# Optimization experiments

Hardware: AMD Instinct MI355X
Metric: run time of the kernel (lower is better)

## Reference

```python
import jax, jax.numpy as jnp
import numpy as np

N_NODES = 500000
D = 128          # input_dim
UNITS = 128
K = 32           # neigh_max
B = 20000        # batch of target nodes
LEAKY_ALPHA = 0.2  # tf.nn.leaky_relu default


def setup_inputs() -> dict:
    key = jax.random.key(0)
    k1, k2, k3, k4, k5, k6, k7 = jax.random.split(key, 7)
    features = jax.random.normal(k1, (N_NODES, D), dtype=jnp.float32)
    node = jax.random.randint(k2, (B, 1), 0, N_NODES, dtype=jnp.int32)
    neighbours = jax.random.randint(k3, (B, K), 0, N_NODES, dtype=jnp.int32)
    # learned parameters (glorot-scale random)
    kernel = jax.random.normal(k4, (1, D, D), dtype=jnp.float32) * (1.0 / np.sqrt(D))
    kernel1 = jax.random.normal(k5, (1, D, D), dtype=jnp.float32) * (1.0 / np.sqrt(D))
    attention_weights = jax.random.normal(k6, (1, 2 * D), dtype=jnp.float32) * (1.0 / np.sqrt(2 * D))
    neigh_weights = jax.random.normal(k7, (D, UNITS), dtype=jnp.float32) * (1.0 / np.sqrt(D))
    return {
        "features": features,
        "node": node,
        "neighbours": neighbours,
        "kernel": kernel,
        "kernel1": kernel1,
        "attention_weights": attention_weights,
        "neigh_weights": neigh_weights,
    }


def reference(features, node, neighbours, kernel, kernel1, attention_weights, neigh_weights):
    # gather: node_feat [B,1,D], neigh_feat [B,K,D]
    node_feat = features[node]
    neigh_feat = features[neighbours]
    # per-node projections (kernel tiled over batch in original == shared matmul)
    node_h = jnp.einsum('bkd,de->bke', node_feat, kernel[0])    # [B,1,D]
    neigh_h = jnp.einsum('bkd,de->bke', neigh_feat, kernel1[0])  # [B,K,D]
    # concat [neigh, tiled node] -> [B,K,2D]
    tile_node = jnp.broadcast_to(node_h, neigh_h.shape)
    concat_feat = jnp.concatenate([neigh_h, tile_node], axis=2)
    # attention score: [B,K,2D] @ [2D,1] -> [B,K,1], leaky_relu (alpha=0.2)
    score = concat_feat @ attention_weights.reshape(2 * D, 1)
    score = jnp.where(score > 0, score, LEAKY_ALPHA * score)
    # softmax over neighbors (axis K)
    final_score = jax.nn.softmax(score, axis=1)                  # [B,K,1]
    # weighted aggregate: neigh_h^T @ score -> [B,D]
    attention_feat = jnp.einsum('bkd,bk->bd', neigh_h, final_score[..., 0])
    # output projection
    return attention_feat @ neigh_weights                        # [B,UNITS]
```

## Files before the change

kernel.cpp:

```cpp
#include <hip/hip_runtime.h>
#include <hip/hip_bf16.h>

#define D 128
#define K 32
#define NB 20000
#define NPB 4
#define NBLK (NB / NPB)
#define NROWS 33
#define FSTR 64

typedef unsigned short u16;
typedef unsigned int   u32;

__device__ inline float blo(u32 v) { return __uint_as_float(v << 16); }
__device__ inline float bhi(u32 v) { return __uint_as_float(v & 0xffff0000u); }
__device__ inline u32 f2b_rne(float x) {
    u32 u = __float_as_uint(x);
    return (u + 0x7fffu + ((u >> 16) & 1u)) >> 16;
}
__device__ inline u32 pack2(float a, float b) { return f2b_rne(a) | (f2b_rne(b) << 16); }

__global__ __launch_bounds__(256)
void precompute_kernel(const float* __restrict__ k0, const float* __restrict__ k1,
                       const float* __restrict__ aw, const float* __restrict__ nw,
                       float* __restrict__ w12, u16* __restrict__ MTb)
{
    int t = threadIdx.x;
    if (blockIdx.x < 64) {
        int gid = blockIdx.x * 256 + t;
        int u = gid & 127, d = gid >> 7;
        float acc = 0.f;
        #pragma unroll 8
        for (int e = 0; e < D; ++e)
            acc = fmaf(k1[d * D + e], nw[e * D + u], acc);
        MTb[u * D + d] = (u16)f2b_rne(acc);
    } else {
        if (t < 128) {
            float acc = 0.f;
            #pragma unroll 8
            for (int e = 0; e < D; ++e)
                acc = fmaf(k1[t * D + e], aw[e], acc);
            w12[t] = acc;
        } else {
            int d = t - 128;
            float acc = 0.f;
            #pragma unroll 8
            for (int e = 0; e < D; ++e)
                acc = fmaf(k0[d * D + e], aw[128 + e], acc);
            w12[t] = acc;
        }
    }
}

__global__ __launch_bounds__(256)
void gat4_kernel(const float* __restrict__ features,
                 const int* __restrict__ node,
                 const int* __restrict__ neigh,
                 const float* __restrict__ w12g,
                 const u16* __restrict__ MTb,
                 float* __restrict__ out)
{
    __shared__ u32   fbuf[128 * FSTR];
    __shared__ float zb[132];
    __shared__ float agg[512];

    const int t  = threadIdx.x;
    const int b4 = blockIdx.x * NPB;
    const int cc = t & 31;
    const int r0 = t >> 5;

    const float4* w4 = (const float4*)w12g;
    const float4 wlo = w4[cc];
    const float4 whi = w4[32 + cc];

    int idx[17];
    #pragma unroll
    for (int i = 0; i < 16; ++i) {
        int r = r0 + 8 * i;
        idx[i] = neigh[(b4 + (r & 3)) * K + (r >> 2)];
    }
    idx[16] = node[b4 + (r0 & 3)];

    const float4* f4 = (const float4*)features;
    float4 v[17];
    #pragma unroll
    for (int i = 0; i < 17; ++i)
        v[i] = f4[(size_t)idx[i] * 32 + cc];

    #pragma unroll
    for (int i = 0; i < 16; ++i) {
        int r = r0 + 8 * i;
        u32* dst = &fbuf[r * FSTR + cc * 2];
        dst[0] = pack2(v[i].x, v[i].y);
        dst[1] = pack2(v[i].z, v[i].w);
        float p = v[i].x * wlo.x + v[i].y * wlo.y + v[i].z * wlo.z + v[i].w * wlo.w;
        p += __shfl_xor(p, 1);
        p += __shfl_xor(p, 2);
        p += __shfl_xor(p, 4);
        p += __shfl_xor(p, 8);
        p += __shfl_xor(p, 16);
        if (cc == 0) zb[(r & 3) * 33 + (r >> 2)] = p;
    }
    if (r0 < 4) {
        float p = v[16].x * whi.x + v[16].y * whi.y + v[16].z * whi.z + v[16].w * whi.w;
        p += __shfl_xor(p, 1);
        p += __shfl_xor(p, 2);
        p += __shfl_xor(p, 4);
        p += __shfl_xor(p, 8);
        p += __shfl_xor(p, 16);
        if (cc == 0) zb[r0 * 33 + 32] = p;
    }
    __syncthreads();

    {
        const int n = t >> 6, l = t & 63, k32 = l & 31;
        float vsc = zb[n * 33 + k32] + zb[n * 33 + 32];
        vsc = vsc > 0.f ? vsc : 0.2f * vsc;
        float m = vsc;
        m = fmaxf(m, __shfl_xor(m, 1));
        m = fmaxf(m, __shfl_xor(m, 2));
        m = fmaxf(m, __shfl_xor(m, 4));
        m = fmaxf(m, __shfl_xor(m, 8));
        m = fmaxf(m, __shfl_xor(m, 16));
        float e = __expf(vsc - m);
        float s = e;
        s += __shfl_xor(s, 1);
        s += __shfl_xor(s, 2);
        s += __shfl_xor(s, 4);
        s += __shfl_xor(s, 8);
        s += __shfl_xor(s, 16);
        const float a = e * (1.0f / s);

        float a0 = 0.f, a1 = 0.f;
        #pragma unroll
        for (int k = 0; k < K; ++k) {
            float al = __shfl(a, k);
            u32 vv = fbuf[(4 * k + n) * FSTR + l];
            a0 = fmaf(al, blo(vv), a0);
            a1 = fmaf(al, bhi(vv), a1);
        }
        agg[n * 128 + 2 * l]     = a0;
        agg[n * 128 + 2 * l + 1] = a1;
    }
    __syncthreads();

    {
        int u  = t & 127;
        int nA = t >> 7;
        const uint4* mrow = (const uint4*)(MTb + u * D);
        const float* aggA = &agg[nA * 128];
        const float* aggB = &agg[(nA + 2) * 128];
        float accA0 = 0.f, accA1 = 0.f, accB0 = 0.f, accB1 = 0.f;
        #pragma unroll
        for (int q = 0; q < 16; ++q) {
            uint4 m4 = mrow[q];
            int d0 = q * 8;
            float m0 = blo(m4.x), m1 = bhi(m4.x), m2 = blo(m4.y), m3 = bhi(m4.y);
            float m4f = blo(m4.z), m5 = bhi(m4.z), m6 = blo(m4.w), m7 = bhi(m4.w);
            accA0 += aggA[d0] * m0 + aggA[d0+1] * m1 + aggA[d0+2] * m2 + aggA[d0+3] * m3;
            accA1 += aggA[d0+4] * m4f + aggA[d0+5] * m5 + aggA[d0+6] * m6 + aggA[d0+7] * m7;
            accB0 += aggB[d0] * m0 + aggB[d0+1] * m1 + aggB[d0+2] * m2 + aggB[d0+3] * m3;
            accB1 += aggB[d0+4] * m4f + aggB[d0+5] * m5 + aggB[d0+6] * m6 + aggB[d0+7] * m7;
        }
        out[(size_t)(b4 + nA) * D + u]     = accA0 + accA1;
        out[(size_t)(b4 + nA + 2) * D + u] = accB0 + accB1;
    }
}

#define RS 33
#define RSF 132
__global__ __launch_bounds__(256)
void gat_fallback_kernel(const float* __restrict__ features, const int* __restrict__ node,
                         const int* __restrict__ neigh,
                         const float* __restrict__ k0, const float* __restrict__ k1,
                         const float* __restrict__ aw, const float* __restrict__ nw,
                         float* __restrict__ out)
{
    __shared__ float4 fbuf[NROWS * RS];
    __shared__ float w1[D], w2[D], h[D];
    __shared__ int   idxs[NROWS];
    __shared__ float psum[NROWS][8];
    __shared__ float zb[NROWS], alpha[K], agg[D];

    const int b = blockIdx.x, t = threadIdx.x;

    if (t < 128) {
        float a = 0.f;
        for (int e = 0; e < D; ++e) a = fmaf(k1[t * D + e], aw[e], a);
        w1[t] = a;
    } else {
        int d = t - 128;
        float a = 0.f;
        for (int e = 0; e < D; ++e) a = fmaf(k0[d * D + e], aw[128 + e], a);
        w2[d] = a;
    }
    if (t < K)       idxs[t] = neigh[b * K + t];
    else if (t == K) idxs[K] = node[b];
    __syncthreads();

    const float4* f4 = (const float4*)features;
    for (int c = t; c < NROWS * 32; c += 256) {
        int j = c >> 5, cc = c & 31;
        fbuf[j * RS + cc] = f4[(size_t)idxs[j] * 32 + cc];
    }
    __syncthreads();

    for (int task = t; task < NROWS * 8; task += 256) {
        int j = task >> 3, sub = task & 7;
        const float* w = (j < K) ? w1 : w2;
        const float4* r = &fbuf[j * RS + sub * 4];
        int d0 = sub * 16;
        float4 a0 = r[0], a1 = r[1], a2 = r[2], a3 = r[3];
        float acc;
        acc  = a0.x * w[d0 + 0]  + a0.y * w[d0 + 1]  + a0.z * w[d0 + 2]  + a0.w * w[d0 + 3];
        acc += a1.x * w[d0 + 4]  + a1.y * w[d0 + 5]  + a1.z * w[d0 + 6]  + a1.w * w[d0 + 7];
        acc += a2.x * w[d0 + 8]  + a2.y * w[d0 + 9]  + a2.z * w[d0 + 10] + a2.w * w[d0 + 11];
        acc += a3.x * w[d0 + 12] + a3.y * w[d0 + 13] + a3.z * w[d0 + 14] + a3.w * w[d0 + 15];
        psum[j][sub] = acc;
    }
    __syncthreads();

    if (t < NROWS) {
        float s = 0.f;
        #pragma unroll
        for (int i = 0; i < 8; ++i) s += psum[t][i];
        zb[t] = s;
    }
    __syncthreads();

    if (t == 0) {
        float c = zb[K];
        float m = -1e30f;
        #pragma unroll
        for (int k = 0; k < K; ++k) {
            float v = zb[k] + c;
            v = v > 0.f ? v : 0.2f * v;
            zb[k] = v;
            m = fmaxf(m, v);
        }
        float s = 0.f;
        #pragma unroll
        for (int k = 0; k < K; ++k) { float e = __expf(zb[k] - m); alpha[k] = e; s += e; }
        float inv = 1.f / s;
        #pragma unroll
        for (int k = 0; k < K; ++k) alpha[k] *= inv;
    }
    __syncthreads();

    const float* fb = (const float*)fbuf;
    if (t < D) {
        float a = 0.f;
        #pragma unroll
        for (int k = 0; k < K; ++k)
            a = fmaf(alpha[k], fb[k * RSF + t], a);
        agg[t] = a;
    }
    __syncthreads();

    if (t < 128) {
        float acc = 0.f;
        for (int d = 0; d < D; ++d) acc = fmaf(agg[d], k1[d * D + t], acc);
        h[t] = acc;
    }
    __syncthreads();
    if (t < 128) {
        float acc = 0.f;
        for (int e = 0; e < D; ++e) acc = fmaf(h[e], nw[e * D + t], acc);
        out[(size_t)b * D + t] = acc;
    }
}

extern "C" void kernel_launch(void* const* d_in, const int* in_sizes, int n_in,
                              void* d_out, int out_size, void* d_ws, size_t ws_size,
                              hipStream_t stream) {
    const float* features = (const float*)d_in[0];
    const int*   node     = (const int*)d_in[1];
    const int*   neigh    = (const int*)d_in[2];
    const float* k0       = (const float*)d_in[3];
    const float* k1       = (const float*)d_in[4];
    const float* aw       = (const float*)d_in[5];
    const float* nw       = (const float*)d_in[6];

    const size_t need = 256 * sizeof(float) + (size_t)D * D * sizeof(u16);
    if (ws_size >= need) {
        float* w12 = (float*)d_ws;
        u16*   MTb = (u16*)(w12 + 256);
        precompute_kernel<<<65, 256, 0, stream>>>(k0, k1, aw, nw, w12, MTb);
        gat4_kernel<<<NBLK, 256, 0, stream>>>(features, node, neigh, w12, MTb,
                                              (float*)d_out);
    } else {
        gat_fallback_kernel<<<NB, 256, 0, stream>>>(features, node, neigh,
                                                    k0, k1, aw, nw, (float*)d_out);
    }
}
```

Before: 385.2 us.

## Make each wavefront own one target node and drop block barriers

Each 64-lane wavefront now handles one target node end to end. Scores, softmax, aggregation and the output projection are all exchanged through wave shuffles rather than shared-memory scratch and __syncthreads. The neighbour gathers are split into two batches of eight loads so the second batch is in flight while the first is packed and reduced. Launch bounds now ask for four blocks per CU. This removes two block-wide barriers and the shared-memory staging, at the cost of many more shuffles in the projection and risk from added register pressure.

```diff
diff --git a/kernel.cpp b/kernel.cpp
--- a/kernel.cpp
+++ b/kernel.cpp
@@ -52,7 +52,7 @@
     }
 }
 
-__global__ __launch_bounds__(256)
+__global__ __launch_bounds__(256, 4)
 void gat4_kernel(const float* __restrict__ features,
                  const int* __restrict__ node,
                  const int* __restrict__ neigh,
@@ -60,111 +60,118 @@
                  const u16* __restrict__ MTb,
                  float* __restrict__ out)
 {
-    __shared__ u32   fbuf[128 * FSTR];
-    __shared__ float zb[132];
-    __shared__ float agg[512];
+    __shared__ u32 fbuf[128 * FSTR];
 
     const int t  = threadIdx.x;
     const int b4 = blockIdx.x * NPB;
-    const int cc = t & 31;
-    const int r0 = t >> 5;
+    const int n  = t >> 6;
+    const int l  = t & 63;
+    const int cc = l & 31;
+    const int h  = l >> 5;
 
     const float4* w4 = (const float4*)w12g;
     const float4 wlo = w4[cc];
     const float4 whi = w4[32 + cc];
 
-    int idx[17];
-    #pragma unroll
-    for (int i = 0; i < 16; ++i) {
-        int r = r0 + 8 * i;
-        idx[i] = neigh[(b4 + (r & 3)) * K + (r >> 2)];
-    }
-    idx[16] = node[b4 + (r0 & 3)];
+    const int idxv = neigh[(b4 + n) * K + cc];
+    const int tidx = node[b4 + n];
 
     const float4* f4 = (const float4*)features;
-    float4 v[17];
-    #pragma unroll
-    for (int i = 0; i < 17; ++i)
-        v[i] = f4[(size_t)idx[i] * 32 + cc];
-
-    #pragma unroll
-    for (int i = 0; i < 16; ++i) {
-        int r = r0 + 8 * i;
+
+    float4 v0[8], v1[8], vt;
+    #pragma unroll
+    for (int i = 0; i < 8; ++i)
+        v0[i] = f4[(size_t)__shfl(idxv, 2 * i + h) * 32 + cc];
+    if (h == 0) vt = f4[(size_t)tidx * 32 + cc];
+
+    float sc = 0.f, sct = 0.f;
+
+    #pragma unroll
+    for (int i = 0; i < 8; ++i) {
+        v1[i] = f4[(size_t)__shfl(idxv, 2 * (i + 8) + h) * 32 + cc];
+        const int r = 4 * (2 * i + h) + n;
         u32* dst = &fbuf[r * FSTR + cc * 2];
-        dst[0] = pack2(v[i].x, v[i].y);
-        dst[1] = pack2(v[i].z, v[i].w);
-        float p = v[i].x * wlo.x + v[i].y * wlo.y + v[i].z * wlo.z + v[i].w * wlo.w;
+        dst[0] = pack2(v0[i].x, v0[i].y);
+        dst[1] = pack2(v0[i].z, v0[i].w);
+        float p = v0[i].x * wlo.x + v0[i].y * wlo.y + v0[i].z * wlo.z + v0[i].w * wlo.w;
         p += __shfl_xor(p, 1);
         p += __shfl_xor(p, 2);
         p += __shfl_xor(p, 4);
         p += __shfl_xor(p, 8);
         p += __shfl_xor(p, 16);
-        if (cc == 0) zb[(r & 3) * 33 + (r >> 2)] = p;
-    }
-    if (r0 < 4) {
-        float p = v[16].x * whi.x + v[16].y * whi.y + v[16].z * whi.z + v[16].w * whi.w;
+        if ((cc >> 1) == i) sc = p;
+    }
+
+    if (h == 0) {
+        float p = vt.x * whi.x + vt.y * whi.y + vt.z * whi.z + vt.w * whi.w;
         p += __shfl_xor(p, 1);
         p += __shfl_xor(p, 2);
         p += __shfl_xor(p, 4);
         p += __shfl_xor(p, 8);
         p += __shfl_xor(p, 16);
-        if (cc == 0) zb[r0 * 33 + 32] = p;
-    }
-    __syncthreads();
-
-    {
-        const int n = t >> 6, l = t & 63, k32 = l & 31;
-        float vsc = zb[n * 33 + k32] + zb[n * 33 + 32];
-        vsc = vsc > 0.f ? vsc : 0.2f * vsc;
-        float m = vsc;
-        m = fmaxf(m, __shfl_xor(m, 1));
-        m = fmaxf(m, __shfl_xor(m, 2));
-        m = fmaxf(m, __shfl_xor(m, 4));
-        m = fmaxf(m, __shfl_xor(m, 8));
-        m = fmaxf(m, __shfl_xor(m, 16));
-        float e = __expf(vsc - m);
-        float s = e;
-        s += __shfl_xor(s, 1);
-        s += __shfl_xor(s, 2);
-        s += __shfl_xor(s, 4);
-        s += __shfl_xor(s, 8);
-        s += __shfl_xor(s, 16);
-        const float a = e * (1.0f / s);
-
-        float a0 = 0.f, a1 = 0.f;
-        #pragma unroll
-        for (int k = 0; k < K; ++k) {
-            float al = __shfl(a, k);
-            u32 vv = fbuf[(4 * k + n) * FSTR + l];
-            a0 = fmaf(al, blo(vv), a0);
-            a1 = fmaf(al, bhi(vv), a1);
-        }
-        agg[n * 128 + 2 * l]     = a0;
-        agg[n * 128 + 2 * l + 1] = a1;
-    }
-    __syncthreads();
-
-    {
-        int u  = t & 127;
-        int nA = t >> 7;
-        const uint4* mrow = (const uint4*)(MTb + u * D);
-        const float* aggA = &agg[nA * 128];
-        const float* aggB = &agg[(nA + 2) * 128];
-        float accA0 = 0.f, accA1 = 0.f, accB0 = 0.f, accB1 = 0.f;
-        #pragma unroll
-        for (int q = 0; q < 16; ++q) {
-            uint4 m4 = mrow[q];
-            int d0 = q * 8;
-            float m0 = blo(m4.x), m1 = bhi(m4.x), m2 = blo(m4.y), m3 = bhi(m4.y);
-            float m4f = blo(m4.z), m5 = bhi(m4.z), m6 = blo(m4.w), m7 = bhi(m4.w);
-            accA0 += aggA[d0] * m0 + aggA[d0+1] * m1 + aggA[d0+2] * m2 + aggA[d0+3] * m3;
-            accA1 += aggA[d0+4] * m4f + aggA[d0+5] * m5 + aggA[d0+6] * m6 + aggA[d0+7] * m7;
-            accB0 += aggB[d0] * m0 + aggB[d0+1] * m1 + aggB[d0+2] * m2 + aggB[d0+3] * m3;
-            accB1 += aggB[d0+4] * m4f + aggB[d0+5] * m5 + aggB[d0+6] * m6 + aggB[d0+7] * m7;
-        }
-        out[(size_t)(b4 + nA) * D + u]     = accA0 + accA1;
-        out[(size_t)(b4 + nA + 2) * D + u] = accB0 + accB1;
-    }
+        sct = p;
+    }
+
+    #pragma unroll
+    for (int i = 0; i < 8; ++i) {
+        const int k = 2 * (i + 8) + h;
+        const int r = 4 * k + n;
+        u32* dst = &fbuf[r * FSTR + cc * 2];
+        dst[0] = pack2(v1[i].x, v1[i].y);
+        dst[1] = pack2(v1[i].z, v1[i].w);
+        float p = v1[i].x * wlo.x + v1[i].y * wlo.y + v1[i].z * wlo.z + v1[i].w * wlo.w;
+        p += __shfl_xor(p, 1);
+        p += __shfl_xor(p, 2);
+        p += __shfl_xor(p, 4);
+        p += __shfl_xor(p, 8);
+        p += __shfl_xor(p, 16);
+        if ((cc >> 1) == i + 8) sc = p;
+    }
+
+    float vsc = __shfl(sc, ((cc & 1) << 5) | cc);
+    vsc += __shfl(sct, 0);
+    vsc = vsc > 0.f ? vsc : 0.2f * vsc;
+    float m = vsc;
+    m = fmaxf(m, __shfl_xor(m, 1));
+    m = fmaxf(m, __shfl_xor(m, 2));
+    m = fmaxf(m, __shfl_xor(m, 4));
+    m = fmaxf(m, __shfl_xor(m, 8));
+    m = fmaxf(m, __shfl_xor(m, 16));
+    float e = __expf(vsc - m);
+    float s = e;
+    s += __shfl_xor(s, 1);
+    s += __shfl_xor(s, 2);
+    s += __shfl_xor(s, 4);
+    s += __shfl_xor(s, 8);
+    s += __shfl_xor(s, 16);
+    const float a = e * (1.0f / s);
+
+    float a0 = 0.f, a1 = 0.f;
+    #pragma unroll
+    for (int k = 0; k < K; ++k) {
+        float al = __shfl(a, k);
+        u32 vv = fbuf[(4 * k + n) * FSTR + l];
+        a0 = fmaf(al, blo(vv), a0);
+        a1 = fmaf(al, bhi(vv), a1);
+    }
+
+    const uint4* mrowA = (const uint4*)(MTb + (size_t)l * D);
+    const uint4* mrowB = (const uint4*)(MTb + (size_t)(l + 64) * D);
+    float accA = 0.f, accB = 0.f;
+    #pragma unroll
+    for (int q = 0; q < 16; ++q) {
+        float g0 = __shfl(a0, 4 * q + 0), g1 = __shfl(a1, 4 * q + 0);
+        float g2 = __shfl(a0, 4 * q + 1), g3 = __shfl(a1, 4 * q + 1);
+        float g4 = __shfl(a0, 4 * q + 2), g5 = __shfl(a1, 4 * q + 2);
+        float g6 = __shfl(a0, 4 * q + 3), g7 = __shfl(a1, 4 * q + 3);
+        uint4 x = mrowA[q], y = mrowB[q];
+        accA += g0 * blo(x.x) + g1 * bhi(x.x) + g2 * blo(x.y) + g3 * bhi(x.y)
+              + g4 * blo(x.z) + g5 * bhi(x.z) + g6 * blo(x.w) + g7 * bhi(x.w);
+        accB += g0 * blo(y.x) + g1 * bhi(y.x) + g2 * blo(y.y) + g3 * bhi(y.y)
+              + g4 * blo(y.z) + g5 * bhi(y.z) + g6 * blo(y.w) + g7 * bhi(y.w);
+    }
+    out[(size_t)(b4 + n) * D + l]      = accA;
+    out[(size_t)(b4 + n) * D + 64 + l] = accB;
 }
 
 #define RS 33
```

Measured after the change: 428.9 us. +11.3%, slower.
